# Kernel tuning notes

Measured on AMD Instinct MI355X. Metric: run time of the kernel, lower is better.

## Reference

```python
import jax, jax.numpy as jnp
import numpy as np

N_NODES = 100000
N_PAIRS = 800000  # undirected pairs; E = 2*N_PAIRS directed edges
D_FEAT = 128
THRESHOLD = 0.01
EPS = 1e-8


def setup_inputs() -> dict:
    key = jax.random.key(0)
    k1, k2, k3, k4 = jax.random.split(key, 4)
    # symmetric edge list without self-loops (each undirected pair in both directions)
    src = jax.random.randint(k1, (N_PAIRS,), 0, N_NODES)
    off = jax.random.randint(k2, (N_PAIRS,), 1, N_NODES)
    dst = (src + off) % N_NODES  # guaranteed != src
    edge_index = jnp.stack([jnp.concatenate([src, dst]),
                            jnp.concatenate([dst, src])]).astype(jnp.int64)
    w_half = jax.random.uniform(k3, (N_PAIRS,), dtype=jnp.float32)
    edge_weight = jnp.concatenate([w_half, w_half])
    features = jax.random.normal(k4, (N_NODES, D_FEAT), dtype=jnp.float32)
    return {"edge_index": edge_index, "edge_weight": edge_weight, "features": features}


def reference(edge_index, edge_weight, features):
    # Cosine-similarity edge dropping (Jaccard.forward, non-binary feature path).
    # Original: build NxN sparse adj, take triu, per-edge cosine sim, zero edges
    # with sim < threshold, symmetrize (triu + triu^T), read back at edge positions.
    # For a symmetric duplicate-free edge list this equals per-edge masking, with
    # diagonal entries doubled by triu + triu^T.
    src, dst = edge_index[0], edge_index[1]
    node_norm = jnp.sqrt(jnp.sum(features * features, axis=-1))  # [N]
    inner = jnp.sum(features[src] * features[dst], axis=-1)       # [E] per-edge gather+dot
    sim = inner / (node_norm[src] * node_norm[dst] + EPS)
    keep = (sim >= THRESHOLD).astype(edge_weight.dtype)
    diag_double = 1.0 + (src == dst).astype(edge_weight.dtype)    # triu+triu^T doubles diagonal
    return edge_weight * keep * diag_double
```

## Files before the change

### kernel.cpp

```cpp
#include <hip/hip_runtime.h>
#include <hip/hip_fp16.h>

#define D_FEAT 128
#define THRESH 0.01f
#define EPS_F  1e-8f

typedef _Float16 half2_t __attribute__((ext_vector_type(2)));


__device__ float edge_out_scalar(const float* __restrict__ feat,
                                 float w, int s, int d) {
#pragma clang fp contract(off)
    const float* fs = feat + (size_t)s * D_FEAT;
    const float* fd = feat + (size_t)d * D_FEAT;
    float r[8], rs[8], rd[8];
#pragma unroll
    for (int j = 0; j < 8; ++j) {
        float a = fs[j], b = fd[j];
        r[j]  = a * b;
        rs[j] = a * a;
        rd[j] = b * b;
    }
    for (int k = 1; k < 16; ++k) {
#pragma unroll
        for (int j = 0; j < 8; ++j) {
            float a = fs[8 * k + j], b = fd[8 * k + j];
            r[j]  = r[j]  + a * b;
            rs[j] = rs[j] + a * a;
            rd[j] = rd[j] + b * b;
        }
    }
    float inner = ((r[0]  + r[1])  + (r[2]  + r[3]))  + ((r[4]  + r[5])  + (r[6]  + r[7]));
    float ss    = ((rs[0] + rs[1]) + (rs[2] + rs[3])) + ((rs[4] + rs[5]) + (rs[6] + rs[7]));
    float dd    = ((rd[0] + rd[1]) + (rd[2] + rd[3])) + ((rd[4] + rd[5]) + (rd[6] + rd[7]));
    float ns = __fsqrt_rn(ss);
    float nd = __fsqrt_rn(dd);
    float denom = ns * nd + EPS_F;
    float sim = inner / denom;
    float keep = (sim >= THRESH) ? 1.0f : 0.0f;
    float diag = (s == d) ? 2.0f : 1.0f;
    return (w * keep) * diag;
}

__device__ __forceinline__ float exact_sim_pairlanes(const float* __restrict__ feat,
                                                     int src, int dst, int h) {
#pragma clang fp contract(off)
    const float4* fs = (const float4*)(feat + (size_t)src * D_FEAT);
    const float4* fd = (const float4*)(feat + (size_t)dst * D_FEAT);
    float r[4], rs[4], rd[4];
    {
        float4 a = fs[h];
        float4 b = fd[h];
        r[0]  = a.x * b.x; r[1]  = a.y * b.y; r[2]  = a.z * b.z; r[3]  = a.w * b.w;
        rs[0] = a.x * a.x; rs[1] = a.y * a.y; rs[2] = a.z * a.z; rs[3] = a.w * a.w;
        rd[0] = b.x * b.x; rd[1] = b.y * b.y; rd[2] = b.z * b.z; rd[3] = b.w * b.w;
    }
#pragma unroll
    for (int k = 1; k < 16; ++k) {
        float4 a = fs[2 * k + h];
        float4 b = fd[2 * k + h];
        r[0]  = r[0]  + a.x * b.x;  r[1]  = r[1]  + a.y * b.y;
        r[2]  = r[2]  + a.z * b.z;  r[3]  = r[3]  + a.w * b.w;
        rs[0] = rs[0] + a.x * a.x;  rs[1] = rs[1] + a.y * a.y;
        rs[2] = rs[2] + a.z * a.z;  rs[3] = rs[3] + a.w * a.w;
        rd[0] = rd[0] + b.x * b.x;  rd[1] = rd[1] + b.y * b.y;
        rd[2] = rd[2] + b.z * b.z;  rd[3] = rd[3] + b.w * b.w;
    }
    float A  = (r[0]  + r[1])  + (r[2]  + r[3]);
    float As = (rs[0] + rs[1]) + (rs[2] + rs[3]);
    float Ad = (rd[0] + rd[1]) + (rd[2] + rd[3]);

    float inner = A  + __shfl_xor(A, 1, 64);
    float ssE   = As + __shfl_xor(As, 1, 64);
    float ddE   = Ad + __shfl_xor(Ad, 1, 64);

    float ns    = __fsqrt_rn(ssE);
    float nd    = __fsqrt_rn(ddE);
    float den   = ns * nd + EPS_F;
    return inner / den;
}

__device__ __forceinline__ float exact_inner_pairlanes(const float* __restrict__ feat,
                                                       int src, int dst, int h) {
#pragma clang fp contract(off)
    const float4* fs = (const float4*)(feat + (size_t)src * D_FEAT);
    const float4* fd = (const float4*)(feat + (size_t)dst * D_FEAT);
    float r[4];
    {
        float4 a = fs[h];
        float4 b = fd[h];
        r[0] = a.x * b.x; r[1] = a.y * b.y; r[2] = a.z * b.z; r[3] = a.w * b.w;
    }
#pragma unroll
    for (int k = 1; k < 16; ++k) {
        float4 a = fs[2 * k + h];
        float4 b = fd[2 * k + h];
        r[0] = r[0] + a.x * b.x;  r[1] = r[1] + a.y * b.y;
        r[2] = r[2] + a.z * b.z;  r[3] = r[3] + a.w * b.w;
    }
    float A = (r[0] + r[1]) + (r[2] + r[3]);
    return A + __shfl_xor(A, 1, 64);
}

__global__ __launch_bounds__(256) void jaccard_edge_kernel(
    const int* __restrict__ ei, const float* __restrict__ w,
    const float* __restrict__ feat, float* __restrict__ out,
    int P, int E)
{
    int t    = blockIdx.x * blockDim.x + threadIdx.x;
    int pair = t >> 1;
    int half = t & 1;
    if (pair >= P) return;

    int src = ei[pair];
    int dst = ei[E + pair];

    float sim  = exact_sim_pairlanes(feat, src, dst, half);
    float keep = (sim >= THRESH) ? 1.0f : 0.0f;

    if (half == 0) {
        float diag = (src == dst) ? 2.0f : 1.0f;
        out[pair] = (w[pair] * keep) * diag;
        int m = P + pair;
        if (m < E) {
            int s2 = ei[m];
            int d2 = ei[E + m];
            if (s2 == dst && d2 == src) out[m] = (w[m] * keep) * diag;
            else                        out[m] = edge_out_scalar(feat, w[m], s2, d2);
        }
    }
}

__global__ __launch_bounds__(256) void norm_convert_kernel(
    const float* __restrict__ feat, __half* __restrict__ hfeat,
    float* __restrict__ nrm, int nNodes)
{
#pragma clang fp contract(off)
    int tid  = blockIdx.x * blockDim.x + threadIdx.x;
    int lane = tid & 63;
    int n    = (tid >> 6) * 16 + (lane >> 2);
    int q    = lane & 3;
    if (n >= nNodes) return;

    const float2* row = (const float2*)(feat + (size_t)n * D_FEAT);
    float2 v[16];
#pragma unroll
    for (int k = 0; k < 16; ++k) v[k] = row[4 * k + q];

    float r0 = v[0].x * v[0].x;
    float r1 = v[0].y * v[0].y;
#pragma unroll
    for (int k = 1; k < 16; ++k) {
        r0 = r0 + v[k].x * v[k].x;
        r1 = r1 + v[k].y * v[k].y;
    }
    float s  = r0 + r1;
    float ss = s + __shfl_xor(s, 1, 64);
    ss       = ss + __shfl_xor(ss, 2, 64);
    float na = __fsqrt_rn(ss);

    bool ok  = isfinite(na) && (na >= 0.03f);
    float r  = ok ? (1.0f / na) : __builtin_nanf("");

    if (q == 0) nrm[n] = na;

    __half* orow = hfeat + (size_t)n * D_FEAT;
#pragma unroll
    for (int k = 0; k < 16; ++k) {
        __half2 h = __floats2half2_rn(v[k].x * r, v[k].y * r);
        *(__half2*)(orow + 8 * k + 2 * q) = h;
    }
}

__device__ __forceinline__ float dot8_f16(uint4 ua, uint4 ub, float acc) {
    acc = __builtin_amdgcn_fdot2(__builtin_bit_cast(half2_t, ua.x),
                                 __builtin_bit_cast(half2_t, ub.x), acc, false);
    acc = __builtin_amdgcn_fdot2(__builtin_bit_cast(half2_t, ua.y),
                                 __builtin_bit_cast(half2_t, ub.y), acc, false);
    acc = __builtin_amdgcn_fdot2(__builtin_bit_cast(half2_t, ua.z),
                                 __builtin_bit_cast(half2_t, ub.z), acc, false);
    acc = __builtin_amdgcn_fdot2(__builtin_bit_cast(half2_t, ua.w),
                                 __builtin_bit_cast(half2_t, ub.w), acc, false);
    return acc;
}

__global__ __launch_bounds__(256) void jaccard_edge_f16u_kernel(
    const int* __restrict__ ei, const float* __restrict__ w,
    const float* __restrict__ feat, const __half* __restrict__ hfeat,
    const float* __restrict__ nrm, float* __restrict__ out, int P, int E)
{
#pragma clang fp contract(off)
    int t    = blockIdx.x * blockDim.x + threadIdx.x;
    int pair = t >> 2;
    int q    = t & 3;
    if (pair >= P) return;

    int src = __builtin_nontemporal_load(ei + pair);
    int dst = __builtin_nontemporal_load(ei + E + pair);

    float wp  = __builtin_nontemporal_load(w + pair);
    int   m   = P + pair;
    bool  hasm = (m < E);
    int s2 = 0, d2 = 0;
    float wm = 0.f;
    if (hasm) {
        s2 = __builtin_nontemporal_load(ei + m);
        d2 = __builtin_nontemporal_load(ei + E + m);
        wm = __builtin_nontemporal_load(w + m);
    }

    const uint4* ha = (const uint4*)(hfeat + (size_t)src * D_FEAT);
    const uint4* hb = (const uint4*)(hfeat + (size_t)dst * D_FEAT);

    uint4 A[4], B[4];
#pragma unroll
    for (int k = 0; k < 4; ++k) {
        A[k] = ha[4 * k + q];
        B[k] = hb[4 * k + q];
    }

    float d = 0.f;
#pragma unroll
    for (int k = 0; k < 4; ++k) d = dot8_f16(A[k], B[k], d);

    d += __shfl_xor(d, 1, 64);
    float dot = d + __shfl_xor(d, 2, 64);

    float diff = dot - THRESH;
    const float bnd = 1.2e-3f;

    float keep;
    if (fabsf(diff) > bnd && fabsf(dot) < 2.0f) {
        keep = (diff >= 0.f) ? 1.0f : 0.0f;
    } else {
        float se = 0.f;
        if (q < 2) {
            float inner = exact_inner_pairlanes(feat, src, dst, q);
            float den   = nrm[src] * nrm[dst] + EPS_F;
            se = inner / den;
        }
        keep = (se >= THRESH) ? 1.0f : 0.0f;
    }

    if (q == 0) {
        float diag = (src == dst) ? 2.0f : 1.0f;
        __builtin_nontemporal_store((wp * keep) * diag, out + pair);
        if (hasm) {
            if (s2 == dst && d2 == src) {
                __builtin_nontemporal_store((wm * keep) * diag, out + m);
            } else {
                out[m] = edge_out_scalar(feat, wm, s2, d2);
            }
        }
    }
}

extern "C" void kernel_launch(void* const* d_in, const int* in_sizes, int n_in,
                              void* d_out, int out_size, void* d_ws, size_t ws_size,
                              hipStream_t stream) {
    const int*   ei   = (const int*)d_in[0];
    const float* w    = (const float*)d_in[1];
    const float* feat = (const float*)d_in[2];
    float*       out  = (float*)d_out;

    int E = in_sizes[1];
    int P = E - E / 2;
    long nfeat = in_sizes[2];
    long nNodes = nfeat / D_FEAT;
    size_t need = (size_t)nfeat * sizeof(__half) + (size_t)nNodes * sizeof(float);

    if (P <= 0) return;

    if (ws_size < need || (nfeat % D_FEAT) != 0) {
        int threads = 2 * P;
        int grid = (threads + 255) / 256;
        jaccard_edge_kernel<<<grid, 256, 0, stream>>>(ei, w, feat, out, P, E);
        return;
    }

    __half* hfeat = (__half*)d_ws;
    float*  nrm   = (float*)((char*)d_ws + (size_t)nfeat * sizeof(__half));

    long nWaves = (nNodes + 15) / 16;
    long tA = nWaves * 64;
    int gridA = (int)((tA + 255) / 256);
    norm_convert_kernel<<<gridA, 256, 0, stream>>>(feat, hfeat, nrm, (int)nNodes);

    int tB = 4 * P;
    jaccard_edge_f16u_kernel<<<(tB + 255) / 256, 256, 0, stream>>>(
        ei, w, feat, hfeat, nrm, out, P, E);
}
```

Measured before the change: 153.9 us.

## Fuse norm conversion and edge pass into one cooperative kernel with grid sync

Moves the per-node normalize/fp16 conversion and the per-pair edge kernel into device functions and runs both phases in one persistent cooperative kernel, separated by a threadfence and a grid-wide sync. The aim is to drop the second kernel launch and the gap between the two dependent launches. In exchange both phases are limited to occupancy-capped grid-stride loops, the fused kernel's register use is set by the heavier phase, and the grid barrier has its own cost. The previous two-launch path is kept as a fallback if the cooperative launch is unsupported or fails.

```diff
diff --git a/kernel.cpp b/kernel.cpp
--- a/kernel.cpp
+++ b/kernel.cpp
@@ -1,5 +1,8 @@
 #include <hip/hip_runtime.h>
 #include <hip/hip_fp16.h>
+#include <hip/hip_cooperative_groups.h>
+
+namespace cg = cooperative_groups;
 
 #define D_FEAT 128
 #define THRESH 0.01f
@@ -102,6 +105,18 @@
     return A + __shfl_xor(A, 1, 64);
 }
 
+__device__ __forceinline__ float dot8_f16(uint4 ua, uint4 ub, float acc) {
+    acc = __builtin_amdgcn_fdot2(__builtin_bit_cast(half2_t, ua.x),
+                                 __builtin_bit_cast(half2_t, ub.x), acc, false);
+    acc = __builtin_amdgcn_fdot2(__builtin_bit_cast(half2_t, ua.y),
+                                 __builtin_bit_cast(half2_t, ub.y), acc, false);
+    acc = __builtin_amdgcn_fdot2(__builtin_bit_cast(half2_t, ua.z),
+                                 __builtin_bit_cast(half2_t, ub.z), acc, false);
+    acc = __builtin_amdgcn_fdot2(__builtin_bit_cast(half2_t, ua.w),
+                                 __builtin_bit_cast(half2_t, ub.w), acc, false);
+    return acc;
+}
+
 __global__ __launch_bounds__(256) void jaccard_edge_kernel(
     const int* __restrict__ ei, const float* __restrict__ w,
     const float* __restrict__ feat, float* __restrict__ out,
@@ -131,17 +146,11 @@
     }
 }
 
-__global__ __launch_bounds__(256) void norm_convert_kernel(
-    const float* __restrict__ feat, __half* __restrict__ hfeat,
-    float* __restrict__ nrm, int nNodes)
-{
-#pragma clang fp contract(off)
-    int tid  = blockIdx.x * blockDim.x + threadIdx.x;
-    int lane = tid & 63;
-    int n    = (tid >> 6) * 16 + (lane >> 2);
-    int q    = lane & 3;
-    if (n >= nNodes) return;
-
+__device__ __forceinline__ void phaseA_node(const float* __restrict__ feat,
+                                            __half* __restrict__ hfeat,
+                                            float* __restrict__ nrm,
+                                            int n, int q) {
+#pragma clang fp contract(off)
     const float2* row = (const float2*)(feat + (size_t)n * D_FEAT);
     float2 v[16];
 #pragma unroll
@@ -172,29 +181,13 @@
     }
 }
 
-__device__ __forceinline__ float dot8_f16(uint4 ua, uint4 ub, float acc) {
-    acc = __builtin_amdgcn_fdot2(__builtin_bit_cast(half2_t, ua.x),
-                                 __builtin_bit_cast(half2_t, ub.x), acc, false);
-    acc = __builtin_amdgcn_fdot2(__builtin_bit_cast(half2_t, ua.y),
-                                 __builtin_bit_cast(half2_t, ub.y), acc, false);
-    acc = __builtin_amdgcn_fdot2(__builtin_bit_cast(half2_t, ua.z),
-                                 __builtin_bit_cast(half2_t, ub.z), acc, false);
-    acc = __builtin_amdgcn_fdot2(__builtin_bit_cast(half2_t, ua.w),
-                                 __builtin_bit_cast(half2_t, ub.w), acc, false);
-    return acc;
-}
-
-__global__ __launch_bounds__(256) void jaccard_edge_f16u_kernel(
+__device__ __forceinline__ void phaseB_pair(
     const int* __restrict__ ei, const float* __restrict__ w,
     const float* __restrict__ feat, const __half* __restrict__ hfeat,
-    const float* __restrict__ nrm, float* __restrict__ out, int P, int E)
-{
-#pragma clang fp contract(off)
-    int t    = blockIdx.x * blockDim.x + threadIdx.x;
-    int pair = t >> 2;
-    int q    = t & 3;
-    if (pair >= P) return;
-
+    const float* __restrict__ nrm, float* __restrict__ out,
+    int pair, int q, int P, int E)
+{
+#pragma clang fp contract(off)
     int src = __builtin_nontemporal_load(ei + pair);
     int dst = __builtin_nontemporal_load(ei + E + pair);
 
@@ -255,6 +248,60 @@
     }
 }
 
+__global__ __launch_bounds__(256) void norm_convert_kernel(
+    const float* __restrict__ feat, __half* __restrict__ hfeat,
+    float* __restrict__ nrm, int nNodes)
+{
+    int tid  = blockIdx.x * blockDim.x + threadIdx.x;
+    int lane = tid & 63;
+    int n    = (tid >> 6) * 16 + (lane >> 2);
+    int q    = lane & 3;
+    if (n >= nNodes) return;
+    phaseA_node(feat, hfeat, nrm, n, q);
+}
+
+__global__ __launch_bounds__(256) void jaccard_edge_f16u_kernel(
+    const int* __restrict__ ei, const float* __restrict__ w,
+    const float* __restrict__ feat, const __half* __restrict__ hfeat,
+    const float* __restrict__ nrm, float* __restrict__ out, int P, int E)
+{
+    int t    = blockIdx.x * blockDim.x + threadIdx.x;
+    int pair = t >> 2;
+    int q    = t & 3;
+    if (pair >= P) return;
+    phaseB_pair(ei, w, feat, hfeat, nrm, out, pair, q, P, E);
+}
+
+__global__ __launch_bounds__(256) void jaccard_fused_kernel(
+    const int* __restrict__ ei, const float* __restrict__ w,
+    const float* __restrict__ feat, __half* __restrict__ hfeat,
+    float* __restrict__ nrm, float* __restrict__ out,
+    int P, int E, int nNodes)
+{
+    cg::grid_group grid = cg::this_grid();
+    long tid0   = (long)blockIdx.x * 256 + threadIdx.x;
+    long stride = (long)gridDim.x * 256;
+
+    long nQuadT = ((long)(nNodes + 15) / 16) * 64;
+    for (long t = tid0; t < nQuadT; t += stride) {
+        int lane = (int)(t & 63);
+        int n    = (int)((t >> 6) * 16 + (lane >> 2));
+        int q    = lane & 3;
+        if (n < nNodes)
+            phaseA_node(feat, hfeat, nrm, n, q);
+    }
+
+    __threadfence();
+    grid.sync();
+
+    long nPairT = (long)4 * P;
+    for (long t = tid0; t < nPairT; t += stride) {
+        int pair = (int)(t >> 2);
+        int q    = (int)(t & 3);
+        phaseB_pair(ei, w, feat, hfeat, nrm, out, pair, q, P, E);
+    }
+}
+
 extern "C" void kernel_launch(void* const* d_in, const int* in_sizes, int n_in,
                               void* d_out, int out_size, void* d_ws, size_t ws_size,
                               hipStream_t stream) {
@@ -280,11 +327,43 @@
 
     __half* hfeat = (__half*)d_ws;
     float*  nrm   = (float*)((char*)d_ws + (size_t)nfeat * sizeof(__half));
+    int nN = (int)nNodes;
+
+    static int coop = -1;
+    static int numCU = 0;
+    static int maxBpc = 0;
+    if (coop < 0) {
+        int dev = 0;
+        hipGetDevice(&dev);
+        int c = 0;
+        hipDeviceGetAttribute(&c, hipDeviceAttributeCooperativeLaunch, dev);
+        hipDeviceGetAttribute(&numCU, hipDeviceAttributeMultiprocessorCount, dev);
+        hipOccupancyMaxActiveBlocksPerMultiprocessor(&maxBpc,
+            (const void*)jaccard_fused_kernel, 256, 0);
+        coop = (c && numCU > 0 && maxBpc > 0) ? 1 : 0;
+    }
+
+    if (coop) {
+        long nQuadT = ((nNodes + 15) / 16) * 64;
+        long needA  = (nQuadT + 255) / 256;
+        long needB  = ((long)4 * P + 255) / 256;
+        long needBl = needA > needB ? needA : needB;
+        long cap    = (long)maxBpc * numCU;
+        long gridF  = needBl < cap ? needBl : cap;
+        if (gridF < 1) gridF = 1;
+
+        void* args[] = {(void*)&ei, (void*)&w, (void*)&feat, (void*)&hfeat,
+                        (void*)&nrm, (void*)&out, (void*)&P, (void*)&E, (void*)&nN};
+        hipError_t err = hipLaunchCooperativeKernel(
+            (const void*)jaccard_fused_kernel, dim3((unsigned)gridF), dim3(256),
+            args, 0, stream);
+        if (err == hipSuccess) return;
+    }
 
     long nWaves = (nNodes + 15) / 16;
     long tA = nWaves * 64;
     int gridA = (int)((tA + 255) / 256);
-    norm_convert_kernel<<<gridA, 256, 0, stream>>>(feat, hfeat, nrm, (int)nNodes);
+    norm_convert_kernel<<<gridA, 256, 0, stream>>>(feat, hfeat, nrm, nN);
 
     int tB = 4 * P;
     jaccard_edge_f16u_kernel<<<(tB + 255) / 256, 256, 0, stream>>>(
```

After: 299.0 us. 1.94x slower.
